# Optimization experiments

Measured on AMD Instinct MI355X. Metric: run time of the kernel, lower is better.

The kernel has to match this reference:

```python
import jax, jax.numpy as jnp
import numpy as np

N_HEADS = 16
K = 8
DILATION = 2
EPS = 1e-6
SCALE = 1.0  # use_qk_norm=True, learn_qk_scale=False -> buffer scale = 1.0


def _dilated_mask(N):
    # allowed[i, j] = (|i-j| <= k*dilation) and ((i-j) % dilation == 0)
    i = jnp.arange(N)[:, None]
    j = jnp.arange(N)[None, :]
    diff = i - j
    return (jnp.abs(diff) <= K * DILATION) & (diff % DILATION == 0)


def setup_inputs() -> dict:
    key = jax.random.key(0)
    k1, k2, k3 = jax.random.split(key, 3)
    B, N, D = 2, 2048, 1024
    x = jax.random.normal(k1, (B, N, D), dtype=jnp.float32)
    w_qkv = jax.random.normal(k2, (3 * D, D), dtype=jnp.float32) * (1.0 / np.sqrt(D))
    b_qkv = jnp.zeros((3 * D,), dtype=jnp.float32)
    w_out = jax.random.normal(k3, (D, D), dtype=jnp.float32) * (1.0 / np.sqrt(D))
    b_out = jnp.zeros((D,), dtype=jnp.float32)
    return {"x": x, "w_qkv": w_qkv, "b_qkv": b_qkv, "w_out": w_out, "b_out": b_out}


def reference(x, w_qkv, b_qkv, w_out, b_out):
    B, N, D = x.shape
    H = N_HEADS
    dh = D // H

    qkv = x @ w_qkv.T + b_qkv                      # [B, N, 3D]
    q, k, v = jnp.split(qkv, 3, axis=-1)
    # [B, N, D] -> [B, H, N, dh]
    q = q.reshape(B, N, H, dh).transpose(0, 2, 1, 3)
    k = k.reshape(B, N, H, dh).transpose(0, 2, 1, 3)
    v = v.reshape(B, N, H, dh).transpose(0, 2, 1, 3)

    # QK-norm
    q = q / (jnp.linalg.norm(q, axis=-1, keepdims=True) + EPS)
    k = k / (jnp.linalg.norm(k, axis=-1, keepdims=True) + EPS)

    scores = jnp.einsum('bhnd,bhmd->bhnm', q, k) * SCALE  # [B, H, N, N]
    allowed = _dilated_mask(N)                              # [N, N] bool
    scores = jnp.where(allowed, scores, -jnp.inf)
    attn = jax.nn.softmax(scores, axis=-1)

    out = jnp.einsum('bhnm,bhmd->bhnd', attn, v)            # [B, H, N, dh]
    out = out.transpose(0, 2, 1, 3).reshape(B, N, D)
    return out @ w_out.T + b_out
```

## Files before the change

### kernel.cpp

```cpp
#include <hip/hip_runtime.h>
#include <hip/hip_bf16.h>
#include <math.h>

typedef __bf16 bf16x8 __attribute__((ext_vector_type(8)));
typedef float f32x4 __attribute__((ext_vector_type(4)));

#define TM 128
#define BK 64

__device__ inline void async16(const void* g, void* l) {
    __builtin_amdgcn_global_load_lds(
        (const __attribute__((address_space(1))) unsigned int*)g,
        (__attribute__((address_space(3))) unsigned int*)l, 16, 0, 0);
}

__device__ inline void stage_sw(__bf16* S, const __bf16* G, int row0, int K, int k0,
                                int tid, int nchunks) {
#pragma unroll
    for (int ci = tid; ci < nchunks; ci += 256) {
        const int r  = ci >> 3;
        const int c  = ci & 7;
        const int cg = c ^ (r & 7);
        const char* g = (const char*)G + ((size_t)(row0 + r) * K + k0 + cg * 8) * 2;
        async16(g, (char*)S + ci * 16);
    }
}

__device__ inline bf16x8 frag_sw(const __bf16* S, int r, int cfrag) {
    const int c = cfrag ^ (r & 7);
    return *(const bf16x8*)(S + r * 64 + c * 8);
}

__global__ __launch_bounds__(256) void cast_mat(
    const float* __restrict__ s0, __bf16* __restrict__ h0, int n0,
    const float* __restrict__ s1, __bf16* __restrict__ h1, int n1,
    const float* __restrict__ s2, __bf16* __restrict__ h2, int n2)
{
    const float* s; __bf16* h; int n;
    if (blockIdx.y == 0)      { s = s0; h = h0; n = n0; }
    else if (blockIdx.y == 1) { s = s1; h = h1; n = n1; }
    else                      { s = s2; h = h2; n = n2; }
    const int base = (blockIdx.x * 256 + threadIdx.x) * 8;
    if (base >= n) return;
    float4 a = ((const float4*)(s + base))[0];
    float4 b = ((const float4*)(s + base))[1];
    float buf[8] = {a.x, a.y, a.z, a.w, b.x, b.y, b.z, b.w};
    bf16x8 hv;
#pragma unroll
    for (int j = 0; j < 8; j++) hv[j] = (__bf16)buf[j];
    *(bf16x8*)(h + base) = hv;
}

__global__ __launch_bounds__(256) void gemm_qkv(
    const __bf16* __restrict__ A, const __bf16* __restrict__ W,
    const float* __restrict__ bias,
    __bf16* __restrict__ q, __bf16* __restrict__ k, __bf16* __restrict__ v,
    int M, int N, int K)
{
    __shared__ __bf16 sA[TM * BK];
    __shared__ __bf16 sW[TM * BK];

    const int tid  = threadIdx.x;
    const int lane = tid & 63;
    const int wave = tid >> 6;
    const int bm = blockIdx.y * TM;
    const int bn = blockIdx.x * 128;
    const int wm = (wave >> 1) * 64;
    const int wn = (wave & 1) * 64;
    const int frow = lane & 15;

    f32x4 acc[4][4] = {};

    for (int k0 = 0; k0 < K; k0 += BK) {
        stage_sw(sA, A, bm, K, k0, tid, TM * 8);
        stage_sw(sW, W, bn, K, k0, tid, TM * 8);
        __syncthreads();

#pragma unroll
        for (int half = 0; half < 2; half++) {
            const int cf = half * 4 + (lane >> 4);
            bf16x8 aF[4], bF[4];
#pragma unroll
            for (int t = 0; t < 4; t++) {
                aF[t] = frag_sw(sA, wm + t * 16 + frow, cf);
                bF[t] = frag_sw(sW, wn + t * 16 + frow, cf);
            }
#pragma unroll
            for (int i = 0; i < 4; i++)
#pragma unroll
                for (int j = 0; j < 4; j++)
                    acc[i][j] = __builtin_amdgcn_mfma_f32_16x16x32_bf16(aF[i], bF[j], acc[i][j], 0, 0, 0);
        }
        __syncthreads();
    }

    const int col0 = bn + wn;
    const int t  = col0 >> 10;
    const int h  = (col0 & 1023) >> 6;

    float bv[4];
#pragma unroll
    for (int j = 0; j < 4; j++) bv[j] = bias[col0 + j * 16 + (lane & 15)];

    float inv_n[4][4];
    if (t < 2) {
#pragma unroll
        for (int i = 0; i < 4; i++)
#pragma unroll
            for (int r = 0; r < 4; r++) {
                float ss = 0.f;
#pragma unroll
                for (int j = 0; j < 4; j++) {
                    float val = acc[i][j][r] + bv[j];
                    ss = fmaf(val, val, ss);
                }
                ss += __shfl_xor(ss, 1);
                ss += __shfl_xor(ss, 2);
                ss += __shfl_xor(ss, 4);
                ss += __shfl_xor(ss, 8);
                inv_n[i][r] = 1.0f / (sqrtf(ss) + 1e-6f);
            }
    }

    __bf16* dstbase = (t == 0) ? q : (t == 1) ? k : v;
#pragma unroll
    for (int i = 0; i < 4; i++) {
        const int gmBase = bm + wm + i * 16 + (lane >> 4) * 4;
#pragma unroll
        for (int j = 0; j < 4; j++) {
            const int dd = (wn & 63) + j * 16 + (lane & 15);
#pragma unroll
            for (int r = 0; r < 4; r++) {
                const int gm = gmBase + r;
                float val = acc[i][j][r] + bv[j];
                if (t < 2) val *= inv_n[i][r];
                const int b  = gm >> 11;
                const int ii = gm & 2047;
                const size_t dst = (((size_t)(b * 16 + h) * 2048) + ii) * 64 + dd;
                dstbase[dst] = (__bf16)val;
            }
        }
    }
}

__global__ __launch_bounds__(256) void gemm_out(
    const __bf16* __restrict__ A, const __bf16* __restrict__ W,
    const float* __restrict__ bias, float* __restrict__ C,
    int M, int N, int K)
{
    __shared__ __bf16 sA[TM * BK];
    __shared__ __bf16 sW[64 * BK];

    const int tid  = threadIdx.x;
    const int lane = tid & 63;
    const int wave = tid >> 6;
    const int bm = blockIdx.y * TM;
    const int bn = blockIdx.x * 64;
    const int wm = (wave >> 1) * 64;
    const int wn = (wave & 1) * 32;
    const int frow = lane & 15;

    f32x4 acc[4][2] = {};

    for (int k0 = 0; k0 < K; k0 += BK) {
        stage_sw(sA, A, bm, K, k0, tid, TM * 8);
        stage_sw(sW, W, bn, K, k0, tid, 64 * 8);
        __syncthreads();

#pragma unroll
        for (int half = 0; half < 2; half++) {
            const int cf = half * 4 + (lane >> 4);
            bf16x8 aF[4], bF[2];
#pragma unroll
            for (int t = 0; t < 4; t++)
                aF[t] = frag_sw(sA, wm + t * 16 + frow, cf);
#pragma unroll
            for (int t = 0; t < 2; t++)
                bF[t] = frag_sw(sW, wn + t * 16 + frow, cf);
#pragma unroll
            for (int i = 0; i < 4; i++)
#pragma unroll
                for (int j = 0; j < 2; j++)
                    acc[i][j] = __builtin_amdgcn_mfma_f32_16x16x32_bf16(aF[i], bF[j], acc[i][j], 0, 0, 0);
        }
        __syncthreads();
    }

#pragma unroll
    for (int i = 0; i < 4; i++) {
        const int gmBase = bm + wm + i * 16 + (lane >> 4) * 4;
#pragma unroll
        for (int j = 0; j < 2; j++) {
            const int gn = bn + wn + j * 16 + (lane & 15);
            const float bvj = bias[gn];
#pragma unroll
            for (int r = 0; r < 4; r++)
                C[(size_t)(gmBase + r) * N + gn] = acc[i][j][r] + bvj;
        }
    }
}

__global__ __launch_bounds__(256) void attn_sparse(
    const __bf16* __restrict__ q, const __bf16* __restrict__ k,
    const __bf16* __restrict__ v, __bf16* __restrict__ ao )
{
    const int wid  = blockIdx.x * 4 + (threadIdx.x >> 6);
    const int lane = threadIdx.x & 63;
    const int g    = lane >> 3;
    const int ld   = (lane & 7) * 8;

    const int bh = wid >> 8;
    const int i  = (wid & 255) * 8 + g;

    const __bf16* qb = q + (size_t)bh * 2048 * 64;
    const __bf16* kb = k + (size_t)bh * 2048 * 64;
    const __bf16* vb = v + (size_t)bh * 2048 * 64;

    bf16x8 qv = *(const bf16x8*)(qb + (size_t)i * 64 + ld);
    float qf[8];
#pragma unroll
    for (int d = 0; d < 8; d++) qf[d] = (float)qv[d];

    float s[17];
#pragma unroll
    for (int t = 0; t < 17; t++) {
        const int j = i + 2 * t - 16;
        const bool valid = (j >= 0) && (j < 2048);
        const int jc = valid ? j : i;
        bf16x8 kv = *(const bf16x8*)(kb + (size_t)jc * 64 + ld);
        float prod = 0.f;
#pragma unroll
        for (int d = 0; d < 8; d++) prod = fmaf(qf[d], (float)kv[d], prod);
        prod += __shfl_xor(prod, 1);
        prod += __shfl_xor(prod, 2);
        prod += __shfl_xor(prod, 4);
        s[t] = valid ? prod : -INFINITY;
    }

    float m = s[0];
#pragma unroll
    for (int t = 1; t < 17; t++) m = fmaxf(m, s[t]);
    float denom = 0.f, p[17];
#pragma unroll
    for (int t = 0; t < 17; t++) { p[t] = __expf(s[t] - m); denom += p[t]; }
    const float inv = 1.0f / denom;

    float a[8] = {};
#pragma unroll
    for (int t = 0; t < 17; t++) {
        const int j = i + 2 * t - 16;
        const int jc = (j >= 0 && j < 2048) ? j : i;
        bf16x8 vv = *(const bf16x8*)(vb + (size_t)jc * 64 + ld);
#pragma unroll
        for (int d = 0; d < 8; d++) a[d] = fmaf(p[t], (float)vv[d], a[d]);
    }

    const int b = bh >> 4, h = bh & 15;
    bf16x8 o;
#pragma unroll
    for (int d = 0; d < 8; d++) o[d] = (__bf16)(a[d] * inv);
    *(bf16x8*)(ao + ((size_t)(b * 2048 + i)) * 1024 + h * 64 + ld) = o;
}

extern "C" void kernel_launch(void* const* d_in, const int* in_sizes, int n_in,
                              void* d_out, int out_size, void* d_ws, size_t ws_size,
                              hipStream_t stream)
{
    const float* x     = (const float*)d_in[0];
    const float* w_qkv = (const float*)d_in[1];
    const float* b_qkv = (const float*)d_in[2];
    const float* w_out = (const float*)d_in[3];
    const float* b_out = (const float*)d_in[4];
    float* out = (float*)d_out;

    const int Dn = 1024;
    const int M  = 4096;
    const int nx = 4194304, nwq = 3145728, nwo = 1048576;

    char* p = (char*)d_ws;
    __bf16* q   = (__bf16*)p;  p += (size_t)nx * 2;
    __bf16* kk  = (__bf16*)p;  p += (size_t)nx * 2;
    __bf16* vv  = (__bf16*)p;  p += (size_t)nx * 2;
    __bf16* xh  = (__bf16*)p;  p += (size_t)nx * 2;
    __bf16* wqh = (__bf16*)p;  p += (size_t)nwq * 2;
    __bf16* woh = (__bf16*)p;  p += (size_t)nwo * 2;
    __bf16* ao  = xh;

    {
        dim3 grid(nx / 8 / 256, 3);
        hipLaunchKernelGGL(cast_mat, grid, dim3(256), 0, stream,
                           x, xh, nx, w_qkv, wqh, nwq, w_out, woh, nwo);
    }
    {
        dim3 grid(3 * Dn / 128, M / TM);
        hipLaunchKernelGGL(gemm_qkv, grid, dim3(256), 0, stream,
                           xh, wqh, b_qkv, q, kk, vv, M, 3 * Dn, Dn);
    }
    hipLaunchKernelGGL(attn_sparse, dim3(65536 / 32), dim3(256), 0, stream,
                       q, kk, vv, ao);
    {
        dim3 grid(Dn / 64, M / TM);
        hipLaunchKernelGGL(gemm_out, grid, dim3(256), 0, stream,
                           ao, woh, b_out, out, M, Dn, Dn);
    }
}
```

Before: 166.7 us.

## Double-buffer GEMM shared tiles with BK=32 to prefetch the next K-slice

```diff
diff --git a/kernel.cpp b/kernel.cpp
--- a/kernel.cpp
+++ b/kernel.cpp
@@ -6,7 +6,6 @@
 typedef float f32x4 __attribute__((ext_vector_type(4)));
 
 #define TM 128
-#define BK 64
 
 __device__ inline void async16(const void* g, void* l) {
     __builtin_amdgcn_global_load_lds(
@@ -14,21 +13,21 @@
         (__attribute__((address_space(3))) unsigned int*)l, 16, 0, 0);
 }
 
-__device__ inline void stage_sw(__bf16* S, const __bf16* G, int row0, int K, int k0,
-                                int tid, int nchunks) {
+__device__ inline void stage32(__bf16* S, const __bf16* G, int row0, int K, int k0,
+                               int tid, int nchunks) {
 #pragma unroll
     for (int ci = tid; ci < nchunks; ci += 256) {
-        const int r  = ci >> 3;
-        const int c  = ci & 7;
-        const int cg = c ^ (r & 7);
+        const int r  = ci >> 2;
+        const int c  = ci & 3;
+        const int cg = c ^ ((r >> 1) & 3);
         const char* g = (const char*)G + ((size_t)(row0 + r) * K + k0 + cg * 8) * 2;
         async16(g, (char*)S + ci * 16);
     }
 }
 
-__device__ inline bf16x8 frag_sw(const __bf16* S, int r, int cfrag) {
-    const int c = cfrag ^ (r & 7);
-    return *(const bf16x8*)(S + r * 64 + c * 8);
+__device__ inline bf16x8 frag32(const __bf16* S, int r, int cfrag) {
+    const int c = cfrag ^ ((r >> 1) & 3);
+    return *(const bf16x8*)(S + r * 32 + c * 8);
 }
 
 __global__ __launch_bounds__(256) void cast_mat(
@@ -57,8 +56,8 @@
     __bf16* __restrict__ q, __bf16* __restrict__ k, __bf16* __restrict__ v,
     int M, int N, int K)
 {
-    __shared__ __bf16 sA[TM * BK];
-    __shared__ __bf16 sW[TM * BK];
+    __shared__ __bf16 sA[2][TM * 32];
+    __shared__ __bf16 sW[2][128 * 32];
 
     const int tid  = threadIdx.x;
     const int lane = tid & 63;
@@ -68,29 +67,32 @@
     const int wm = (wave >> 1) * 64;
     const int wn = (wave & 1) * 64;
     const int frow = lane & 15;
+    const int cf   = lane >> 4;
 
     f32x4 acc[4][4] = {};
 
-    for (int k0 = 0; k0 < K; k0 += BK) {
-        stage_sw(sA, A, bm, K, k0, tid, TM * 8);
-        stage_sw(sW, W, bn, K, k0, tid, TM * 8);
-        __syncthreads();
-
-#pragma unroll
-        for (int half = 0; half < 2; half++) {
-            const int cf = half * 4 + (lane >> 4);
-            bf16x8 aF[4], bF[4];
-#pragma unroll
-            for (int t = 0; t < 4; t++) {
-                aF[t] = frag_sw(sA, wm + t * 16 + frow, cf);
-                bF[t] = frag_sw(sW, wn + t * 16 + frow, cf);
-            }
-#pragma unroll
-            for (int i = 0; i < 4; i++)
-#pragma unroll
-                for (int j = 0; j < 4; j++)
-                    acc[i][j] = __builtin_amdgcn_mfma_f32_16x16x32_bf16(aF[i], bF[j], acc[i][j], 0, 0, 0);
-        }
+    stage32(sA[0], A, bm, K, 0, tid, TM * 4);
+    stage32(sW[0], W, bn, K, 0, tid, 128 * 4);
+    __syncthreads();
+
+    const int NIT = K / 32;
+    for (int it = 0; it < NIT; it++) {
+        const int cur = it & 1;
+        if (it + 1 < NIT) {
+            stage32(sA[cur ^ 1], A, bm, K, (it + 1) * 32, tid, TM * 4);
+            stage32(sW[cur ^ 1], W, bn, K, (it + 1) * 32, tid, 128 * 4);
+        }
+        bf16x8 aF[4], bF[4];
+#pragma unroll
+        for (int t = 0; t < 4; t++) {
+            aF[t] = frag32(sA[cur], wm + t * 16 + frow, cf);
+            bF[t] = frag32(sW[cur], wn + t * 16 + frow, cf);
+        }
+#pragma unroll
+        for (int i = 0; i < 4; i++)
+#pragma unroll
+            for (int j = 0; j < 4; j++)
+                acc[i][j] = __builtin_amdgcn_mfma_f32_16x16x32_bf16(aF[i], bF[j], acc[i][j], 0, 0, 0);
         __syncthreads();
     }
 
@@ -148,8 +150,8 @@
     const float* __restrict__ bias, float* __restrict__ C,
     int M, int N, int K)
 {
-    __shared__ __bf16 sA[TM * BK];
-    __shared__ __bf16 sW[64 * BK];
+    __shared__ __bf16 sA[2][TM * 32];
+    __shared__ __bf16 sW[2][64 * 32];
 
     const int tid  = threadIdx.x;
     const int lane = tid & 63;
@@ -159,30 +161,33 @@
     const int wm = (wave >> 1) * 64;
     const int wn = (wave & 1) * 32;
     const int frow = lane & 15;
+    const int cf   = lane >> 4;
 
     f32x4 acc[4][2] = {};
 
-    for (int k0 = 0; k0 < K; k0 += BK) {
-        stage_sw(sA, A, bm, K, k0, tid, TM * 8);
-        stage_sw(sW, W, bn, K, k0, tid, 64 * 8);
-        __syncthreads();
-
-#pragma unroll
-        for (int half = 0; half < 2; half++) {
-            const int cf = half * 4 + (lane >> 4);
-            bf16x8 aF[4], bF[2];
-#pragma unroll
-            for (int t = 0; t < 4; t++)
-                aF[t] = frag_sw(sA, wm + t * 16 + frow, cf);
-#pragma unroll
-            for (int t = 0; t < 2; t++)
-                bF[t] = frag_sw(sW, wn + t * 16 + frow, cf);
-#pragma unroll
-            for (int i = 0; i < 4; i++)
-#pragma unroll
-                for (int j = 0; j < 2; j++)
-                    acc[i][j] = __builtin_amdgcn_mfma_f32_16x16x32_bf16(aF[i], bF[j], acc[i][j], 0, 0, 0);
-        }
+    stage32(sA[0], A, bm, K, 0, tid, TM * 4);
+    stage32(sW[0], W, bn, K, 0, tid, 64 * 4);
+    __syncthreads();
+
+    const int NIT = K / 32;
+    for (int it = 0; it < NIT; it++) {
+        const int cur = it & 1;
+        if (it + 1 < NIT) {
+            stage32(sA[cur ^ 1], A, bm, K, (it + 1) * 32, tid, TM * 4);
+            stage32(sW[cur ^ 1], W, bn, K, (it + 1) * 32, tid, 64 * 4);
+        }
+        bf16x8 aF[4], bF[2];
+#pragma unroll
+        for (int t = 0; t < 4; t++)
+            aF[t] = frag32(sA[cur], wm + t * 16 + frow, cf);
+#pragma unroll
+        for (int t = 0; t < 2; t++)
+            bF[t] = frag32(sW[cur], wn + t * 16 + frow, cf);
+#pragma unroll
+        for (int i = 0; i < 4; i++)
+#pragma unroll
+            for (int j = 0; j < 2; j++)
+                acc[i][j] = __builtin_amdgcn_mfma_f32_16x16x32_bf16(aF[i], bF[j], acc[i][j], 0, 0, 0);
         __syncthreads();
     }
 
```

Result: slower. 181.8 us (+9.0%).
